# Performance work log

Hardware: AMD Instinct MI355X
Metric: run time of the kernel (lower is better)

## Reference

```python
import jax, jax.numpy as jnp
import numpy as np

HEADS = 16

def setup_inputs() -> dict:
    key = jax.random.key(0)
    k1, k2, k3, k4 = jax.random.split(key, 4)
    B, T, S, W = 2, 2048, 2048, 1024
    x = jax.random.normal(k1, (B, T, W), dtype=jnp.float32)
    cond_k = jax.random.normal(k2, (B, S, W), dtype=jnp.float32)
    cond_v = jax.random.normal(k3, (B, S, W), dtype=jnp.float32)
    w_proj = jax.random.normal(k4, (W, W), dtype=jnp.float32) * 0.02
    b_proj = jnp.zeros((W,), dtype=jnp.float32)
    return {"x": x, "cond_k": cond_k, "cond_v": cond_v, "w_proj": w_proj, "b_proj": b_proj}

def reference(x, cond_k, cond_v, w_proj, b_proj):
    B, T, W = x.shape
    S = cond_k.shape[1]
    H = HEADS
    d = W // H
    scale = 1.0 / jnp.sqrt(jnp.sqrt(jnp.float32(d)))  # applied to both q and k
    q = x.reshape(B, T, H, d) * scale
    k = cond_k.reshape(B, S, H, d) * scale
    v = cond_v.reshape(B, S, H, d)
    # scores: [B, H, T, S]
    scores = jnp.einsum('bthd,bshd->bhts', q, k)
    w = jax.nn.softmax(scores.astype(jnp.float32), axis=-1).astype(scores.dtype)
    out = jnp.einsum('bhts,bshd->bthd', w, v).reshape(B, T, W)
    # c_proj: torch Linear -> x @ W.T + b
    return out @ w_proj.T + b_proj
```

## Files before the change

### kernel.cpp

```cpp
#include <hip/hip_runtime.h>

#define Bn 2
#define Hn 16
#define Tn 2048
#define Sn 2048
#define Wd 1024
#define Dh 64

typedef __attribute__((ext_vector_type(8))) short s16x8;
typedef __attribute__((ext_vector_type(4))) short s16x4;
typedef __attribute__((ext_vector_type(4))) float f32x4;
typedef __attribute__((ext_vector_type(4))) unsigned u32x4;

#define MFMA(a, b, c) __builtin_amdgcn_mfma_f32_16x16x32_bf16((a), (b), (c), 0, 0, 0)

__device__ __forceinline__ s16x8 ld8(const short* p) { return *(const s16x8*)p; }

__device__ __forceinline__ short f2bf(float f) {
    unsigned u = __builtin_bit_cast(unsigned, f);
    u += 0x7FFFu + ((u >> 16) & 1u);
    return (short)(u >> 16);
}

__device__ __forceinline__ unsigned cvtpk(float lo, float hi) {
    unsigned r;
    asm("v_cvt_pk_bf16_f32 %0, %1, %2" : "=v"(r) : "v"(lo), "v"(hi));
    return r;
}

__global__ __launch_bounds__(256) void prep(const float* __restrict__ ck,
                                            const float* __restrict__ cv,
                                            const float* __restrict__ wp,
                                            short* __restrict__ kp,
                                            short* __restrict__ vp,
                                            short* __restrict__ wb)
{
    __shared__ short T[64][72];
    const int blk = blockIdx.x;
    const int tid = threadIdx.x;
    if (blk < 2048) {
        const int isV = blk >> 10;
        const int c   = blk & 1023;
        const int bh = c >> 5, sc = c & 31;
        const int b = bh >> 4, h = bh & 15;
        const float* src = (isV ? cv : ck) + (size_t)(b * Sn + sc * 64) * Wd + h * Dh;
#pragma unroll
        for (int i = 0; i < 4; ++i) {
            int f = i * 256 + tid, sr = f >> 4, c4 = f & 15;
            float4 v = *(const float4*)(src + (size_t)sr * Wd + c4 * 4);
            s16x4 o;
            o[0] = f2bf(v.x); o[1] = f2bf(v.y); o[2] = f2bf(v.z); o[3] = f2bf(v.w);
            *(s16x4*)&T[sr][c4 * 4] = o;
        }
        __syncthreads();
        const int rt = tid >> 6;
        const int l = tid & 63, quad = l >> 4, l16 = l & 15;
        if (!isV) {
            size_t base = ((size_t)((bh * 128 + sc * 4 + rt) * 2)) * 512 + l * 8;
            *(s16x8*)(kp + base)       = *(const s16x8*)&T[rt * 16 + l16][quad * 8];
            *(s16x8*)(kp + base + 512) = *(const s16x8*)&T[rt * 16 + l16][32 + quad * 8];
        } else {
#pragma unroll
            for (int g = 0; g < 2; ++g) {
                s16x8 o;
#pragma unroll
                for (int j = 0; j < 8; ++j) {
                    int s = 32 * g + 16 * (j >> 2) + quad * 4 + (j & 3);
                    o[j] = T[s][rt * 16 + l16];
                }
                *(s16x8*)(vp + ((size_t)((bh * 32 + sc) * 8 + rt * 2 + g)) * 512 + l * 8) = o;
            }
        }
    } else {
        int i = ((blk - 2048) * 256 + tid) * 8;
        float4 a = *(const float4*)(wp + i);
        float4 b = *(const float4*)(wp + i + 4);
        s16x8 o;
        o[0] = f2bf(a.x); o[1] = f2bf(a.y); o[2] = f2bf(a.z); o[3] = f2bf(a.w);
        o[4] = f2bf(b.x); o[5] = f2bf(b.y); o[6] = f2bf(b.z); o[7] = f2bf(b.w);
        *(s16x8*)(wb + i) = o;
    }
}

__global__ __launch_bounds__(256, 2) void attn_fused(
    const float* __restrict__ x, const short* __restrict__ kp,
    const short* __restrict__ vt, short* __restrict__ ao)
{
    const int tid  = threadIdx.x;
    const int w    = tid >> 6;
    const int l    = tid & 63;
    const int quad = l >> 4;
    const int l16  = l & 15;

    const int bh = blockIdx.x & 31;
    const int qt = blockIdx.x >> 5;
    const int b  = bh >> 4, h = bh & 15;

    const int qrow0 = qt * 128 + w * 32;

    const float SQ = 0.125f * 1.4426950408889634f;
    s16x8 aq[2][2];
#pragma unroll
    for (int mi = 0; mi < 2; ++mi)
#pragma unroll
        for (int c = 0; c < 2; ++c) {
            const float* p = x + (size_t)(b * Tn + qrow0 + mi * 16 + l16) * Wd
                               + h * Dh + c * 32 + quad * 8;
            float4 a = ((const float4*)p)[0], bb = ((const float4*)p)[1];
            s16x8 o;
            o[0] = f2bf(a.x * SQ); o[1] = f2bf(a.y * SQ); o[2] = f2bf(a.z * SQ); o[3] = f2bf(a.w * SQ);
            o[4] = f2bf(bb.x * SQ); o[5] = f2bf(bb.y * SQ); o[6] = f2bf(bb.z * SQ); o[7] = f2bf(bb.w * SQ);
            aq[mi][c] = o;
        }

    f32x4 oacc[2][4], dnacc[2];
#pragma unroll
    for (int mi = 0; mi < 2; ++mi) {
#pragma unroll
        for (int nt = 0; nt < 4; ++nt) {
            oacc[mi][nt][0] = 0.f; oacc[mi][nt][1] = 0.f;
            oacc[mi][nt][2] = 0.f; oacc[mi][nt][3] = 0.f;
        }
        dnacc[mi][0] = 0.f; dnacc[mi][1] = 0.f; dnacc[mi][2] = 0.f; dnacc[mi][3] = 0.f;
    }

    s16x8 ones;
#pragma unroll
    for (int j = 0; j < 8; ++j) ones[j] = (short)0x3F80;

    const short* kp_h = kp + (size_t)bh * 131072;
    const short* vp_h = vt + (size_t)bh * 131072;

    const f32x4 z = {0.f, 0.f, 0.f, 0.f};
    const int NIT = Sn / 64;

    s16x8 kfA[4][2], kfB[4][2];
#pragma unroll
    for (int sj = 0; sj < 4; ++sj)
#pragma unroll
        for (int g = 0; g < 2; ++g)
            kfA[sj][g] = ld8(kp_h + ((size_t)(sj * 2 + g)) * 512 + l * 8);

#define BODY(KF, KN, itv)                                                       \
    do {                                                                        \
        if ((itv) + 1 < NIT) {                                                  \
            _Pragma("unroll") for (int sj = 0; sj < 4; ++sj)                    \
                _Pragma("unroll") for (int g = 0; g < 2; ++g)                   \
                    KN[sj][g] = ld8(kp_h +                                      \
                        ((size_t)(((itv) + 1) * 8 + sj * 2 + g)) * 512 + l * 8);\
        }                                                                       \
        s16x8 vf[4][2];                                                         \
        _Pragma("unroll") for (int nt = 0; nt < 4; ++nt)                        \
            _Pragma("unroll") for (int g = 0; g < 2; ++g)                       \
                vf[nt][g] = ld8(vp_h +                                          \
                    ((size_t)((itv) * 8 + nt * 2 + g)) * 512 + l * 8);          \
        f32x4 sc[2][4];                                                         \
        __builtin_amdgcn_s_setprio(1);                                          \
        _Pragma("unroll") for (int sj = 0; sj < 4; ++sj)                        \
            _Pragma("unroll") for (int mi = 0; mi < 2; ++mi) {                  \
                sc[mi][sj] = MFMA(KF[sj][0], aq[mi][0], z);                     \
                sc[mi][sj] = MFMA(KF[sj][1], aq[mi][1], sc[mi][sj]);            \
            }                                                                   \
        __builtin_amdgcn_s_setprio(0);                                          \
        s16x8 ap[2][2];                                                         \
        _Pragma("unroll") for (int mi = 0; mi < 2; ++mi) {                      \
            float ex[4][4];                                                     \
            _Pragma("unroll") for (int sj = 0; sj < 4; ++sj)                    \
                _Pragma("unroll") for (int r = 0; r < 4; ++r)                   \
                    ex[sj][r] = __builtin_amdgcn_exp2f(sc[mi][sj][r]);          \
            _Pragma("unroll") for (int g = 0; g < 2; ++g) {                     \
                u32x4 pk;                                                       \
                pk[0] = cvtpk(ex[2 * g][0],     ex[2 * g][1]);                  \
                pk[1] = cvtpk(ex[2 * g][2],     ex[2 * g][3]);                  \
                pk[2] = cvtpk(ex[2 * g + 1][0], ex[2 * g + 1][1]);              \
                pk[3] = cvtpk(ex[2 * g + 1][2], ex[2 * g + 1][3]);              \
                ap[mi][g] = __builtin_bit_cast(s16x8, pk);                      \
            }                                                                   \
        }                                                                       \
        __builtin_amdgcn_s_setprio(1);                                          \
        _Pragma("unroll") for (int mi = 0; mi < 2; ++mi) {                      \
            dnacc[mi] = MFMA(ap[mi][0], ones, dnacc[mi]);                       \
            dnacc[mi] = MFMA(ap[mi][1], ones, dnacc[mi]);                       \
        }                                                                       \
        _Pragma("unroll") for (int mi = 0; mi < 2; ++mi)                        \
            _Pragma("unroll") for (int nt = 0; nt < 4; ++nt) {                  \
                oacc[mi][nt] = MFMA(ap[mi][0], vf[nt][0], oacc[mi][nt]);        \
                oacc[mi][nt] = MFMA(ap[mi][1], vf[nt][1], oacc[mi][nt]);        \
            }                                                                   \
        __builtin_amdgcn_s_setprio(0);                                          \
    } while (0)

    for (int it = 0; it < NIT; it += 2) {
        BODY(kfA, kfB, it);
        BODY(kfB, kfA, it + 1);
    }
#undef BODY

#pragma unroll
    for (int mi = 0; mi < 2; ++mi)
#pragma unroll
        for (int r = 0; r < 4; ++r) {
            float inv = 1.0f / dnacc[mi][r];
            int t = qrow0 + mi * 16 + quad * 4 + r;
#pragma unroll
            for (int nt = 0; nt < 4; ++nt)
                ao[(size_t)(b * Tn + t) * Wd + h * Dh + nt * 16 + l16] =
                    f2bf(oacc[mi][nt][r] * inv);
        }
}

#define LSTR 40

__global__ __launch_bounds__(256, 2) void proj_gemm(
    const short* __restrict__ A, const short* __restrict__ Wb,
    const float* __restrict__ bias, float* __restrict__ out)
{
    __shared__ alignas(16) short As[2][128 * LSTR];
    __shared__ alignas(16) short Bs[2][64 * LSTR];

    const int tid  = threadIdx.x;
    const int w    = tid >> 6;
    const int l    = tid & 63;
    const int quad = l >> 4;
    const int l16  = l & 15;

    const int bn = blockIdx.x & 15;
    const int bm = blockIdx.x >> 4;
    const int m0 = bm * 128;
    const int n0 = bn * 64;
    const int wm = (w & 1) * 64;
    const int wn = (w >> 1) * 32;

    const int rr = tid >> 2;
    const int sg = tid & 3;

    f32x4 acc[4][2];
#pragma unroll
    for (int mi = 0; mi < 4; ++mi)
#pragma unroll
        for (int nt = 0; nt < 2; ++nt) {
            acc[mi][nt][0] = 0.f; acc[mi][nt][1] = 0.f;
            acc[mi][nt][2] = 0.f; acc[mi][nt][3] = 0.f;
        }

    s16x8 ra0 = ld8(A  + (size_t)(m0 + rr) * Wd + sg * 8);
    s16x8 ra1 = ld8(A  + (size_t)(m0 + 64 + rr) * Wd + sg * 8);
    s16x8 rb  = ld8(Wb + (size_t)(n0 + rr) * Wd + sg * 8);
    *(s16x8*)&As[0][rr * LSTR + sg * 8]        = ra0;
    *(s16x8*)&As[0][(rr + 64) * LSTR + sg * 8] = ra1;
    *(s16x8*)&Bs[0][rr * LSTR + sg * 8]        = rb;
    __syncthreads();

    for (int k0 = 0; k0 < Wd; k0 += 32) {
        const int p = (k0 >> 5) & 1;

        if (k0 + 32 < Wd) {
            ra0 = ld8(A  + (size_t)(m0 + rr) * Wd + k0 + 32 + sg * 8);
            ra1 = ld8(A  + (size_t)(m0 + 64 + rr) * Wd + k0 + 32 + sg * 8);
            rb  = ld8(Wb + (size_t)(n0 + rr) * Wd + k0 + 32 + sg * 8);
        }

        s16x8 a[4], bw[2];
#pragma unroll
        for (int mi = 0; mi < 4; ++mi)
            a[mi] = *(const s16x8*)&As[p][(wm + mi * 16 + l16) * LSTR + quad * 8];
#pragma unroll
        for (int nt = 0; nt < 2; ++nt)
            bw[nt] = *(const s16x8*)&Bs[p][(wn + nt * 16 + l16) * LSTR + quad * 8];
        __builtin_amdgcn_s_setprio(1);
#pragma unroll
        for (int mi = 0; mi < 4; ++mi)
#pragma unroll
            for (int nt = 0; nt < 2; ++nt)
                acc[mi][nt] = MFMA(a[mi], bw[nt], acc[mi][nt]);
        __builtin_amdgcn_s_setprio(0);

        if (k0 + 32 < Wd) {
            *(s16x8*)&As[p ^ 1][rr * LSTR + sg * 8]        = ra0;
            *(s16x8*)&As[p ^ 1][(rr + 64) * LSTR + sg * 8] = ra1;
            *(s16x8*)&Bs[p ^ 1][rr * LSTR + sg * 8]        = rb;
        }
        __syncthreads();
    }

#pragma unroll
    for (int nt = 0; nt < 2; ++nt) {
        float bv = bias[n0 + wn + nt * 16 + l16];
#pragma unroll
        for (int mi = 0; mi < 4; ++mi)
#pragma unroll
            for (int r = 0; r < 4; ++r)
                out[(size_t)(m0 + wm + mi * 16 + quad * 4 + r) * Wd + n0 + wn + nt * 16 + l16] =
                    acc[mi][nt][r] + bv;
    }
}

extern "C" void kernel_launch(void* const* d_in, const int* in_sizes, int n_in,
                              void* d_out, int out_size, void* d_ws, size_t ws_size,
                              hipStream_t stream) {
    const float* x  = (const float*)d_in[0];
    const float* ck = (const float*)d_in[1];
    const float* cv = (const float*)d_in[2];
    const float* wp = (const float*)d_in[3];
    const float* bp = (const float*)d_in[4];

    const int nX = Bn * Tn * Wd;
    const int nW = Wd * Wd;

    short* kpb = (short*)d_ws;
    short* vpb = kpb + nX;
    short* wbb = vpb + nX;
    short* am  = wbb + nW;

    prep<<<dim3(2048 + nW / 2048), dim3(256), 0, stream>>>(ck, cv, wp, kpb, vpb, wbb);

    attn_fused<<<dim3(Bn * Hn * (Tn / 128)), dim3(256), 0, stream>>>(x, kpb, vpb, am);
    proj_gemm<<<dim3((Bn * Tn / 128) * (Wd / 64)), dim3(256), 0, stream>>>(
        am, wbb, bp, (float*)d_out);
}
```

Measured before the change: 155.9 us.

## Stage K/V tiles through LDS with double-buffered global_load_lds

Rather than having every wave load the K and V fragments straight from global memory into registers, the block now cooperatively copies each 64-key K/V tile into double-buffered LDS using global_load_lds, and each wave reads its fragments from LDS. This is meant to remove the four-fold redundant global/L2 traffic across the block's waves and to prefetch the next tile asynchronously. In exchange it adds a barrier plus a full vmcnt wait on every iteration and 32KB of LDS per block, which may limit occupancy and overlap.

```diff
diff --git a/kernel.cpp b/kernel.cpp
--- a/kernel.cpp
+++ b/kernel.cpp
@@ -26,6 +26,12 @@
     unsigned r;
     asm("v_cvt_pk_bf16_f32 %0, %1, %2" : "=v"(r) : "v"(lo), "v"(hi));
     return r;
+}
+
+__device__ __forceinline__ void gl_lds(const short* g, short* lds) {
+    __builtin_amdgcn_global_load_lds(
+        (const __attribute__((address_space(1))) void*)g,
+        (__attribute__((address_space(3))) void*)lds, 16, 0, 0);
 }
 
 __global__ __launch_bounds__(256) void prep(const float* __restrict__ ck,
@@ -86,6 +92,9 @@
     const float* __restrict__ x, const short* __restrict__ kp,
     const short* __restrict__ vt, short* __restrict__ ao)
 {
+    __shared__ alignas(16) short Ks[2][8 * 512];
+    __shared__ alignas(16) short Vs[2][8 * 512];
+
     const int tid  = threadIdx.x;
     const int w    = tid >> 6;
     const int l    = tid & 63;
@@ -97,6 +106,18 @@
     const int b  = bh >> 4, h = bh & 15;
 
     const int qrow0 = qt * 128 + w * 32;
+
+    const short* kp_h = kp + (size_t)bh * 131072;
+    const short* vp_h = vt + (size_t)bh * 131072;
+
+    const int f0 = w * 2;
+
+#pragma unroll
+    for (int f2 = 0; f2 < 2; ++f2) {
+        int f = f0 + f2;
+        gl_lds(kp_h + (size_t)f * 512 + l * 8, &Ks[0][f * 512]);
+        gl_lds(vp_h + (size_t)f * 512 + l * 8, &Vs[0][f * 512]);
+    }
 
     const float SQ = 0.125f * 1.4426950408889634f;
     s16x8 aq[2][2];
@@ -128,73 +149,88 @@
 #pragma unroll
     for (int j = 0; j < 8; ++j) ones[j] = (short)0x3F80;
 
-    const short* kp_h = kp + (size_t)bh * 131072;
-    const short* vp_h = vt + (size_t)bh * 131072;
-
     const f32x4 z = {0.f, 0.f, 0.f, 0.f};
     const int NIT = Sn / 64;
 
-    s16x8 kfA[4][2], kfB[4][2];
-#pragma unroll
-    for (int sj = 0; sj < 4; ++sj)
-#pragma unroll
-        for (int g = 0; g < 2; ++g)
-            kfA[sj][g] = ld8(kp_h + ((size_t)(sj * 2 + g)) * 512 + l * 8);
-
-#define BODY(KF, KN, itv)                                                       \
-    do {                                                                        \
-        if ((itv) + 1 < NIT) {                                                  \
-            _Pragma("unroll") for (int sj = 0; sj < 4; ++sj)                    \
-                _Pragma("unroll") for (int g = 0; g < 2; ++g)                   \
-                    KN[sj][g] = ld8(kp_h +                                      \
-                        ((size_t)(((itv) + 1) * 8 + sj * 2 + g)) * 512 + l * 8);\
-        }                                                                       \
-        s16x8 vf[4][2];                                                         \
-        _Pragma("unroll") for (int nt = 0; nt < 4; ++nt)                        \
-            _Pragma("unroll") for (int g = 0; g < 2; ++g)                       \
-                vf[nt][g] = ld8(vp_h +                                          \
-                    ((size_t)((itv) * 8 + nt * 2 + g)) * 512 + l * 8);          \
-        f32x4 sc[2][4];                                                         \
-        __builtin_amdgcn_s_setprio(1);                                          \
-        _Pragma("unroll") for (int sj = 0; sj < 4; ++sj)                        \
-            _Pragma("unroll") for (int mi = 0; mi < 2; ++mi) {                  \
-                sc[mi][sj] = MFMA(KF[sj][0], aq[mi][0], z);                     \
-                sc[mi][sj] = MFMA(KF[sj][1], aq[mi][1], sc[mi][sj]);            \
-            }                                                                   \
-        __builtin_amdgcn_s_setprio(0);                                          \
-        s16x8 ap[2][2];                                                         \
-        _Pragma("unroll") for (int mi = 0; mi < 2; ++mi) {                      \
-            float ex[4][4];                                                     \
-            _Pragma("unroll") for (int sj = 0; sj < 4; ++sj)                    \
-                _Pragma("unroll") for (int r = 0; r < 4; ++r)                   \
-                    ex[sj][r] = __builtin_amdgcn_exp2f(sc[mi][sj][r]);          \
-            _Pragma("unroll") for (int g = 0; g < 2; ++g) {                     \
-                u32x4 pk;                                                       \
-                pk[0] = cvtpk(ex[2 * g][0],     ex[2 * g][1]);                  \
-                pk[1] = cvtpk(ex[2 * g][2],     ex[2 * g][3]);                  \
-                pk[2] = cvtpk(ex[2 * g + 1][0], ex[2 * g + 1][1]);              \
-                pk[3] = cvtpk(ex[2 * g + 1][2], ex[2 * g + 1][3]);              \
-                ap[mi][g] = __builtin_bit_cast(s16x8, pk);                      \
-            }                                                                   \
-        }                                                                       \
-        __builtin_amdgcn_s_setprio(1);                                          \
-        _Pragma("unroll") for (int mi = 0; mi < 2; ++mi) {                      \
-            dnacc[mi] = MFMA(ap[mi][0], ones, dnacc[mi]);                       \
-            dnacc[mi] = MFMA(ap[mi][1], ones, dnacc[mi]);                       \
-        }                                                                       \
-        _Pragma("unroll") for (int mi = 0; mi < 2; ++mi)                        \
-            _Pragma("unroll") for (int nt = 0; nt < 4; ++nt) {                  \
-                oacc[mi][nt] = MFMA(ap[mi][0], vf[nt][0], oacc[mi][nt]);        \
-                oacc[mi][nt] = MFMA(ap[mi][1], vf[nt][1], oacc[mi][nt]);        \
-            }                                                                   \
-        __builtin_amdgcn_s_setprio(0);                                          \
-    } while (0)
-
-    for (int it = 0; it < NIT; it += 2) {
-        BODY(kfA, kfB, it);
-        BODY(kfB, kfA, it + 1);
-    }
-#undef BODY
+    asm volatile("s_waitcnt vmcnt(0)" ::: "memory");
+    __syncthreads();
+
+    for (int it = 0; it < NIT; ++it) {
+        const int p = it & 1;
+
+        if (it + 1 < NIT) {
+            const size_t cbase = (size_t)(it + 1) * 8;
+#pragma unroll
+            for (int f2 = 0; f2 < 2; ++f2) {
+                int f = f0 + f2;
+                gl_lds(kp_h + (cbase + f) * 512 + l * 8, &Ks[p ^ 1][f * 512]);
+                gl_lds(vp_h + (cbase + f) * 512 + l * 8, &Vs[p ^ 1][f * 512]);
+            }
+        }
+
+        s16x8 kf[4][2];
+#pragma unroll
+        for (int sj = 0; sj < 4; ++sj)
+#pragma unroll
+            for (int g = 0; g < 2; ++g)
+                kf[sj][g] = *(const s16x8*)&Ks[p][(sj * 2 + g) * 512 + l * 8];
+
+        f32x4 sc[2][4];
+        __builtin_amdgcn_s_setprio(1);
+#pragma unroll
+        for (int sj = 0; sj < 4; ++sj)
+#pragma unroll
+            for (int mi = 0; mi < 2; ++mi) {
+                sc[mi][sj] = MFMA(kf[sj][0], aq[mi][0], z);
+                sc[mi][sj] = MFMA(kf[sj][1], aq[mi][1], sc[mi][sj]);
+            }
+        __builtin_amdgcn_s_setprio(0);
+
+        s16x8 ap[2][2];
+#pragma unroll
+        for (int mi = 0; mi < 2; ++mi) {
+            float ex[4][4];
+#pragma unroll
+            for (int sj = 0; sj < 4; ++sj)
+#pragma unroll
+                for (int r = 0; r < 4; ++r)
+                    ex[sj][r] = __builtin_amdgcn_exp2f(sc[mi][sj][r]);
+#pragma unroll
+            for (int g = 0; g < 2; ++g) {
+                u32x4 pk;
+                pk[0] = cvtpk(ex[2 * g][0],     ex[2 * g][1]);
+                pk[1] = cvtpk(ex[2 * g][2],     ex[2 * g][3]);
+                pk[2] = cvtpk(ex[2 * g + 1][0], ex[2 * g + 1][1]);
+                pk[3] = cvtpk(ex[2 * g + 1][2], ex[2 * g + 1][3]);
+                ap[mi][g] = __builtin_bit_cast(s16x8, pk);
+            }
+        }
+
+        s16x8 vf[4][2];
+#pragma unroll
+        for (int nt = 0; nt < 4; ++nt)
+#pragma unroll
+            for (int g = 0; g < 2; ++g)
+                vf[nt][g] = *(const s16x8*)&Vs[p][(nt * 2 + g) * 512 + l * 8];
+
+        __builtin_amdgcn_s_setprio(1);
+#pragma unroll
+        for (int mi = 0; mi < 2; ++mi) {
+            dnacc[mi] = MFMA(ap[mi][0], ones, dnacc[mi]);
+            dnacc[mi] = MFMA(ap[mi][1], ones, dnacc[mi]);
+        }
+#pragma unroll
+        for (int mi = 0; mi < 2; ++mi)
+#pragma unroll
+            for (int nt = 0; nt < 4; ++nt) {
+                oacc[mi][nt] = MFMA(ap[mi][0], vf[nt][0], oacc[mi][nt]);
+                oacc[mi][nt] = MFMA(ap[mi][1], vf[nt][1], oacc[mi][nt]);
+            }
+        __builtin_amdgcn_s_setprio(0);
+
+        asm volatile("s_waitcnt vmcnt(0)" ::: "memory");
+        __syncthreads();
+    }
 
 #pragma unroll
     for (int mi = 0; mi < 2; ++mi)
```

Result: no change. 153.0 us (-1.9%).
